# Kernel tuning notes

Measured on AMD Instinct MI355X. Metric: run time of the kernel, lower is better.

## Reference

```python
import jax, jax.numpy as jnp
import numpy as np

V, E, H, O = 50000, 300, 1024, 5
B, T = 64, 512


def setup_inputs() -> dict:
    key = jax.random.key(0)
    ks = jax.random.split(key, 8)
    s_ih = 1.0 / np.sqrt(H)
    return {
        "x": jax.random.randint(ks[0], (B, T), 0, V, dtype=jnp.int32),
        "embeddings": jax.random.normal(ks[1], (V, E), dtype=jnp.float32),
        "W_ih": jax.random.uniform(ks[2], (3 * H, E), jnp.float32, -s_ih, s_ih),
        "W_hh": jax.random.uniform(ks[3], (3 * H, H), jnp.float32, -s_ih, s_ih),
        "b_ih": jax.random.uniform(ks[4], (3 * H,), jnp.float32, -s_ih, s_ih),
        "b_hh": jax.random.uniform(ks[5], (3 * H,), jnp.float32, -s_ih, s_ih),
        "W_fc": jax.random.uniform(ks[6], (O, H), jnp.float32, -s_ih, s_ih),
        "b_fc": jax.random.uniform(ks[7], (O,), jnp.float32, -s_ih, s_ih),
    }


def _gru_last_hidden(emb, W_ih, W_hh, b_ih, b_hh):
    # emb: [B, T, E] -> last hidden state [B, H]
    Hd = W_hh.shape[1]
    # Precompute input contributions for all timesteps: [B, T, 3H]
    gx_all = jnp.einsum("bte,ge->btg", emb, W_ih) + b_ih
    gx_all = jnp.swapaxes(gx_all, 0, 1)  # [T, B, 3H] for scan

    def step(h, gx):
        gh = h @ W_hh.T + b_hh  # [B, 3H]
        xr, xz, xn = jnp.split(gx, 3, axis=-1)
        hr, hz, hn = jnp.split(gh, 3, axis=-1)
        r = jax.nn.sigmoid(xr + hr)
        z = jax.nn.sigmoid(xz + hz)
        n = jnp.tanh(xn + r * hn)
        h_new = (1.0 - z) * n + z * h
        return h_new, None

    h0 = jnp.zeros((emb.shape[0], Hd), dtype=emb.dtype)
    h_last, _ = jax.lax.scan(step, h0, gx_all)
    return h_last


def reference(x, embeddings, W_ih, W_hh, b_ih, b_hh, W_fc, b_fc):
    emb = embeddings[x]  # [B, T, E] embedding lookup (frozen table)
    h_last = _gru_last_hidden(emb, W_ih, W_hh, b_ih, b_hh)  # [B, H]
    return h_last @ W_fc.T + b_fc  # [B, O]
```

## Files before the change

kernel.cpp:

```cpp
#include <hip/hip_runtime.h>
#include <hip/hip_bf16.h>

typedef unsigned short u16;
typedef unsigned long long u64;
typedef __attribute__((ext_vector_type(8))) short bf16x8;
typedef __attribute__((ext_vector_type(4))) float f32x4;

#define MFMA16(a, b, c) __builtin_amdgcn_mfma_f32_16x16x32_bf16((a), (b), (c), 0, 0, 0)

static constexpr int Ee = 300, EP = 320, Hh = 1024, G3 = 3072;
static constexpr int Bb = 64, Tt = 512;

static constexpr long OFF_GX   = 0L;
static constexpr long OFF_EMB  = 201326592L;
static constexpr long OFF_WIH  = 222298112L;
static constexpr long OFF_WHH  = 224264192L;
static constexpr long OFF_HBUF = 230555648L;
static constexpr long OFF_FLAG = 230817792L;

__device__ __forceinline__ u16 f2bf(float f) {
    union { float f; unsigned u; } v; v.f = f;
    unsigned u = v.u;
    return (u16)((u + 0x7fffu + ((u >> 16) & 1u)) >> 16);
}
__device__ __forceinline__ float bf2f(u16 u) {
    union { unsigned u; float f; } v; v.u = ((unsigned)u) << 16;
    return v.f;
}
__device__ __forceinline__ float fast_sigmoid(float x) {
    return 1.f / (1.f + __expf(-x));
}
__device__ __forceinline__ float fast_tanh(float x) {
    float ax = fabsf(x);
    float e = __expf(-2.f * ax);
    float t = (1.f - e) / (1.f + e);
    return copysignf(t, x);
}

static constexpr long R0 = (long)Bb * Tt * EP;
static constexpr long R1 = (long)G3 * EP;
static constexpr long R2 = (long)G3 * Hh;
static constexpr long R3 = 131072;
static constexpr long R4 = 4096;
static constexpr long R5 = 320;

__global__ void prep_kernel(const int* __restrict__ x, const float* __restrict__ emb,
                            const float* __restrict__ wih, const float* __restrict__ whh,
                            const float* __restrict__ bfc,
                            u16* __restrict__ emb_bf, u16* __restrict__ wih_bf,
                            u16* __restrict__ whh_bf, u16* __restrict__ h0,
                            int* __restrict__ flags, float* __restrict__ out) {
    const long total = R0 + R1 + R2 + R3 + R4 + R5;
    for (long i = (long)blockIdx.x * blockDim.x + threadIdx.x; i < total;
         i += (long)gridDim.x * blockDim.x) {
        if (i < R0) {
            const int m = (int)(i / EP), k = (int)(i % EP);
            const int b = m & 63, t = m >> 6;
            u16 v = 0;
            if (k < Ee) {
                const int xi = x[b * Tt + t];
                v = f2bf(emb[(size_t)xi * Ee + k]);
            }
            emb_bf[i] = v;
        } else if (i < R0 + R1) {
            const long j = i - R0;
            const int k = (int)(j % EP);
            const int n = (int)(j / EP);
            wih_bf[j] = (k < Ee) ? f2bf(wih[(size_t)n * Ee + k]) : (u16)0;
        } else if (i < R0 + R1 + R2) {
            const long j = i - R0 - R1;
            whh_bf[j] = f2bf(whh[j]);
        } else if (i < R0 + R1 + R2 + R3) {
            h0[i - R0 - R1 - R2] = 0;
        } else if (i < R0 + R1 + R2 + R3 + R4) {
            flags[i - R0 - R1 - R2 - R3] = 0;
        } else {
            const long j = i - R0 - R1 - R2 - R3 - R4;
            out[j] = bfc[j % 5];
        }
    }
}

__global__ __launch_bounds__(256, 2)
void gx_gemm(const u16* __restrict__ A, const u16* __restrict__ Bm,
             const float* __restrict__ bih, u16* __restrict__ gx) {
    __shared__ __align__(16) u16 lA[128 * 32];
    __shared__ __align__(16) u16 lB[128 * 32];
    const int tid = threadIdx.x;
    const int lane = tid & 63;
    const int wv = tid >> 6;
    const int quad = lane >> 4, l15 = lane & 15;
    const int m0 = blockIdx.x * 128;
    const int n0 = blockIdx.y * 128;
    const int mo = (wv & 1) * 64, no = (wv >> 1) * 64;
    const int srow = tid >> 2;
    const int sseg = tid & 3;

    f32x4 acc[4][4] = {};

    for (int s = 0; s < 10; ++s) {
        const int k0 = s * 32;
        __syncthreads();
#pragma unroll
        for (int p = 0; p < 2; ++p) {
            const u16* ga = A + (size_t)(m0 + p * 64 + srow) * EP + k0 + sseg * 8;
            u16* la = &lA[p * 2048 + wv * 512];
            __builtin_amdgcn_global_load_lds(
                (const __attribute__((address_space(1))) void*)ga,
                (__attribute__((address_space(3))) void*)la, 16, 0, 0);
            const u16* gb = Bm + (size_t)(n0 + p * 64 + srow) * EP + k0 + sseg * 8;
            u16* lb = &lB[p * 2048 + wv * 512];
            __builtin_amdgcn_global_load_lds(
                (const __attribute__((address_space(1))) void*)gb,
                (__attribute__((address_space(3))) void*)lb, 16, 0, 0);
        }
        __syncthreads();

        bf16x8 af[4], bfr[4];
#pragma unroll
        for (int mt = 0; mt < 4; ++mt)
            af[mt] = *(const bf16x8*)&lA[(mo + mt * 16 + l15) * 32 + quad * 8];
#pragma unroll
        for (int nt = 0; nt < 4; ++nt)
            bfr[nt] = *(const bf16x8*)&lB[(no + nt * 16 + l15) * 32 + quad * 8];
#pragma unroll
        for (int mt = 0; mt < 4; ++mt)
#pragma unroll
            for (int nt = 0; nt < 4; ++nt)
                acc[mt][nt] = MFMA16(af[mt], bfr[nt], acc[mt][nt]);
    }

#pragma unroll
    for (int mt = 0; mt < 4; ++mt) {
        const int mg = m0 + mo + mt * 16 + quad * 4;
        const int t = mg >> 6, b0 = mg & 63;
#pragma unroll
        for (int nt = 0; nt < 4; ++nt) {
            const int n = n0 + no + nt * 16 + l15;
            const float bi = bih[n];
            ushort4 vv;
            vv.x = f2bf(acc[mt][nt][0] + bi);
            vv.y = f2bf(acc[mt][nt][1] + bi);
            vv.z = f2bf(acc[mt][nt][2] + bi);
            vv.w = f2bf(acc[mt][nt][3] + bi);
            *(ushort4*)&gx[((size_t)t * G3 + n) * 64 + b0] = vv;
        }
    }
}

__global__ __launch_bounds__(512, 2)
void scan_kernel(const u16* __restrict__ whh, const float* __restrict__ bhh,
                 const u16* __restrict__ gx, u16* __restrict__ hbuf,
                 const float* __restrict__ wfc, float* __restrict__ out,
                 int* __restrict__ flags) {
    __shared__ __align__(16) u16 lh[16 * 1032];
    __shared__ __align__(16) float red[2][3][4][16 * 20];

    const int bid = blockIdx.x;
    const int bg = bid >> 5;
    const int cg = bid & 31;
    const int w = threadIdx.x >> 6;
    const int lane = threadIdx.x & 63;
    const int kq = w & 3;
    const int nh = w >> 2;
    const int quad = lane >> 4, l15 = lane & 15;
    const int c0 = cg * 32;
    const bool isGate = (w == 3) || (w == 4);
    const int gnh = (w == 3) ? 0 : 1;

    bf16x8 wf[3][8];
#pragma unroll
    for (int g = 0; g < 3; ++g) {
        const size_t rbase = (size_t)(g * 1024 + c0 + nh * 16 + l15) * 1024;
#pragma unroll
        for (int s = 0; s < 8; ++s)
            wf[g][s] = *(const bf16x8*)&whh[rbase + (kq * 8 + s) * 32 + quad * 8];
    }

    float bh[3][4];
    u16 gxv[3][4];
    float hO[4] = {0.f, 0.f, 0.f, 0.f};
    if (isGate) {
#pragma unroll
        for (int g = 0; g < 3; ++g)
#pragma unroll
            for (int jj = 0; jj < 4; ++jj) {
                const int jglob = c0 + gnh * 16 + quad * 4 + jj;
                bh[g][jj] = bhh[g * 1024 + jglob];
                gxv[g][jj] = gx[((size_t)g * 1024 + jglob) * 64 + bg * 16 + l15];
            }
    }

    u64* hbq = (u64*)hbuf + (size_t)bg * 8192;
    int* gflag = &flags[(bg * 64 + lane) * 16];
    int* myflag = &flags[(bg * 64 + cg * 2 + gnh) * 16];
    const int srow = threadIdx.x >> 5;
    const int scol = threadIdx.x & 31;
    u64* lhq = (u64*)lh;

    for (int t = 0; t < 512; ++t) {
        const u64* hcq = hbq + (t & 1) * 4096;
        u16* hn = hbuf + (size_t)bg * 32768 + ((t + 1) & 1) * 16384;

        {
            int v = __hip_atomic_load(gflag, __ATOMIC_RELAXED, __HIP_MEMORY_SCOPE_AGENT);
            bool done = (v >= t);
            while (!__all(done)) {
                __builtin_amdgcn_s_sleep(1);
                if (!done) {
                    v = __hip_atomic_load(gflag, __ATOMIC_RELAXED, __HIP_MEMORY_SCOPE_AGENT);
                    done = (v >= t);
                }
            }
            __asm__ volatile("" ::: "memory");
        }

        u64 stg[8];
#pragma unroll
        for (int r = 0; r < 8; ++r)
            stg[r] = __hip_atomic_load(&hcq[srow * 256 + scol + 32 * r],
                                       __ATOMIC_RELAXED, __HIP_MEMORY_SCOPE_AGENT);
#pragma unroll
        for (int r = 0; r < 8; ++r)
            lhq[srow * 258 + scol + 32 * r] = stg[r];
        __syncthreads();

        bf16x8 af[8];
#pragma unroll
        for (int s = 0; s < 8; ++s)
            af[s] = *(const bf16x8*)&lh[l15 * 1032 + kq * 256 + s * 32 + quad * 8];
        f32x4 acc[3] = {};
#pragma unroll
        for (int s = 0; s < 8; ++s) {
            acc[0] = MFMA16(af[s], wf[0][s], acc[0]);
            acc[1] = MFMA16(af[s], wf[1][s], acc[1]);
            acc[2] = MFMA16(af[s], wf[2][s], acc[2]);
        }
#pragma unroll
        for (int g = 0; g < 3; ++g)
#pragma unroll
            for (int r = 0; r < 4; ++r)
                red[nh][g][kq][(quad * 4 + r) * 20 + l15] = acc[g][r];
        __syncthreads();

        if (isGate) {
            f32x4 rr[3][4];
#pragma unroll
            for (int g = 0; g < 3; ++g)
#pragma unroll
                for (int k = 0; k < 4; ++k)
                    rr[g][k] = *(const f32x4*)&red[gnh][g][k][l15 * 20 + quad * 4];
            u64 pack = 0;
#pragma unroll
            for (int jj = 0; jj < 4; ++jj) {
                const float s0 = rr[0][0][jj] + rr[0][1][jj] + rr[0][2][jj] + rr[0][3][jj];
                const float s1 = rr[1][0][jj] + rr[1][1][jj] + rr[1][2][jj] + rr[1][3][jj];
                const float s2 = rr[2][0][jj] + rr[2][1][jj] + rr[2][2][jj] + rr[2][3][jj];
                const float rg = fast_sigmoid(bf2f(gxv[0][jj]) + s0 + bh[0][jj]);
                const float zg = fast_sigmoid(bf2f(gxv[1][jj]) + s1 + bh[1][jj]);
                const float ng = fast_tanh(bf2f(gxv[2][jj]) + rg * (s2 + bh[2][jj]));
                const float hv = (1.f - zg) * ng + zg * hO[jj];
                hO[jj] = hv;
                pack |= (u64)f2bf(hv) << (jj * 16);
            }
            if (t < 511) {
                __hip_atomic_store((u64*)&hn[l15 * 1024 + c0 + gnh * 16 + quad * 4],
                                   pack, __ATOMIC_RELAXED, __HIP_MEMORY_SCOPE_AGENT);
                __builtin_amdgcn_s_waitcnt(0);
                if (lane == 0)
                    __hip_atomic_store(myflag, t + 1, __ATOMIC_RELAXED,
                                       __HIP_MEMORY_SCOPE_AGENT);
#pragma unroll
                for (int g = 0; g < 3; ++g)
#pragma unroll
                    for (int jj = 0; jj < 4; ++jj)
                        gxv[g][jj] = gx[((size_t)(t + 1) * G3 + g * 1024 + c0 +
                                         gnh * 16 + quad * 4 + jj) * 64 + bg * 16 + l15];
            }
        }
    }

    if (isGate) {
#pragma unroll
        for (int p = 0; p < 5; ++p) {
            float v = 0.f;
#pragma unroll
            for (int jj = 0; jj < 4; ++jj)
                v += hO[jj] * wfc[p * 1024 + c0 + gnh * 16 + quad * 4 + jj];
            v += __shfl_xor(v, 16);
            v += __shfl_xor(v, 32);
            if (quad == 0)
                atomicAdd(&out[(bg * 16 + l15) * 5 + p], v);
        }
    }
}

extern "C" void kernel_launch(void* const* d_in, const int* in_sizes, int n_in,
                              void* d_out, int out_size, void* d_ws, size_t ws_size,
                              hipStream_t stream) {
    const int*   x   = (const int*)d_in[0];
    const float* emb = (const float*)d_in[1];
    const float* wih = (const float*)d_in[2];
    const float* whh = (const float*)d_in[3];
    const float* bih = (const float*)d_in[4];
    const float* bhh = (const float*)d_in[5];
    const float* wfc = (const float*)d_in[6];
    const float* bfc = (const float*)d_in[7];
    float* out = (float*)d_out;

    char* ws = (char*)d_ws;
    u16*   gxw   = (u16*)(ws + OFF_GX);
    u16*   embbf = (u16*)(ws + OFF_EMB);
    u16*   wihbf = (u16*)(ws + OFF_WIH);
    u16*   whhbf = (u16*)(ws + OFF_WHH);
    u16*   hbuf  = (u16*)(ws + OFF_HBUF);
    int*   flags = (int*)(ws + OFF_FLAG);

    prep_kernel<<<8192, 256, 0, stream>>>(x, emb, wih, whh, bfc, embbf, wihbf,
                                          whhbf, hbuf, flags, out);

    gx_gemm<<<dim3(256, 24), 256, 0, stream>>>(embbf, wihbf, bih, gxw);

    scan_kernel<<<128, 512, 0, stream>>>(whhbf, bhh, gxw, hbuf, wfc, out, flags);
}
```

Baseline: 2.103 ms.

## Replace per-step flag barrier with timestep-tagged hidden-state words

Removes the separate flag array and its spin-wait. Each hidden value is now stored as a 32-bit word holding the bf16 value and the timestep tag, and consumers poll the data itself with coherent wide loads until every tag matches. This drops the store→waitcnt→flag-store→flag-load round trip from the critical serial path of the recurrence. In exchange the hidden-state traffic doubles and the tag/compare work runs on every poll.

```diff
diff --git a/kernel.cpp b/kernel.cpp
--- a/kernel.cpp
+++ b/kernel.cpp
@@ -2,9 +2,11 @@
 #include <hip/hip_bf16.h>
 
 typedef unsigned short u16;
+typedef unsigned int u32;
 typedef unsigned long long u64;
 typedef __attribute__((ext_vector_type(8))) short bf16x8;
 typedef __attribute__((ext_vector_type(4))) float f32x4;
+typedef __attribute__((ext_vector_type(4))) unsigned int u32x4;
 
 #define MFMA16(a, b, c) __builtin_amdgcn_mfma_f32_16x16x32_bf16((a), (b), (c), 0, 0, 0)
 
@@ -16,7 +18,6 @@
 static constexpr long OFF_WIH  = 222298112L;
 static constexpr long OFF_WHH  = 224264192L;
 static constexpr long OFF_HBUF = 230555648L;
-static constexpr long OFF_FLAG = 230817792L;
 
 __device__ __forceinline__ u16 f2bf(float f) {
     union { float f; unsigned u; } v; v.f = f;
@@ -41,16 +42,15 @@
 static constexpr long R1 = (long)G3 * EP;
 static constexpr long R2 = (long)G3 * Hh;
 static constexpr long R3 = 131072;
-static constexpr long R4 = 4096;
 static constexpr long R5 = 320;
 
 __global__ void prep_kernel(const int* __restrict__ x, const float* __restrict__ emb,
                             const float* __restrict__ wih, const float* __restrict__ whh,
                             const float* __restrict__ bfc,
                             u16* __restrict__ emb_bf, u16* __restrict__ wih_bf,
-                            u16* __restrict__ whh_bf, u16* __restrict__ h0,
-                            int* __restrict__ flags, float* __restrict__ out) {
-    const long total = R0 + R1 + R2 + R3 + R4 + R5;
+                            u16* __restrict__ whh_bf, u32* __restrict__ h32,
+                            float* __restrict__ out) {
+    const long total = R0 + R1 + R2 + R3 + R5;
     for (long i = (long)blockIdx.x * blockDim.x + threadIdx.x; i < total;
          i += (long)gridDim.x * blockDim.x) {
         if (i < R0) {
@@ -71,11 +71,10 @@
             const long j = i - R0 - R1;
             whh_bf[j] = f2bf(whh[j]);
         } else if (i < R0 + R1 + R2 + R3) {
-            h0[i - R0 - R1 - R2] = 0;
-        } else if (i < R0 + R1 + R2 + R3 + R4) {
-            flags[i - R0 - R1 - R2 - R3] = 0;
+            const long j = i - R0 - R1 - R2;
+            h32[j] = ((j >> 14) & 1) ? 0xFFFFu : 0u;
         } else {
-            const long j = i - R0 - R1 - R2 - R3 - R4;
+            const long j = i - R0 - R1 - R2 - R3;
             out[j] = bfc[j % 5];
         }
     }
@@ -150,17 +149,17 @@
 
 __global__ __launch_bounds__(512, 2)
 void scan_kernel(const u16* __restrict__ whh, const float* __restrict__ bhh,
-                 const u16* __restrict__ gx, u16* __restrict__ hbuf,
-                 const float* __restrict__ wfc, float* __restrict__ out,
-                 int* __restrict__ flags) {
+                 const u16* __restrict__ gx, u32* __restrict__ hball,
+                 const float* __restrict__ wfc, float* __restrict__ out) {
     __shared__ __align__(16) u16 lh[16 * 1032];
     __shared__ __align__(16) float red[2][3][4][16 * 20];
 
     const int bid = blockIdx.x;
     const int bg = bid >> 5;
     const int cg = bid & 31;
-    const int w = threadIdx.x >> 6;
-    const int lane = threadIdx.x & 63;
+    const int tid = threadIdx.x;
+    const int w = tid >> 6;
+    const int lane = tid & 63;
     const int kq = w & 3;
     const int nh = w >> 2;
     const int quad = lane >> 4, l15 = lane & 15;
@@ -191,38 +190,72 @@
             }
     }
 
-    u64* hbq = (u64*)hbuf + (size_t)bg * 8192;
-    int* gflag = &flags[(bg * 64 + lane) * 16];
-    int* myflag = &flags[(bg * 64 + cg * 2 + gnh) * 16];
-    const int srow = threadIdx.x >> 5;
-    const int scol = threadIdx.x & 31;
+    u32* hb = hball + (size_t)bg * 32768;
     u64* lhq = (u64*)lh;
+    const int t4 = tid << 2;
+    const int srow0 = tid >> 8;
+    const int sc4 = tid & 255;
 
     for (int t = 0; t < 512; ++t) {
-        const u64* hcq = hbq + (t & 1) * 4096;
-        u16* hn = hbuf + (size_t)bg * 32768 + ((t + 1) & 1) * 16384;
-
-        {
-            int v = __hip_atomic_load(gflag, __ATOMIC_RELAXED, __HIP_MEMORY_SCOPE_AGENT);
-            bool done = (v >= t);
-            while (!__all(done)) {
-                __builtin_amdgcn_s_sleep(1);
-                if (!done) {
-                    v = __hip_atomic_load(gflag, __ATOMIC_RELAXED, __HIP_MEMORY_SCOPE_AGENT);
-                    done = (v >= t);
-                }
-            }
-            __asm__ volatile("" ::: "memory");
-        }
-
-        u64 stg[8];
-#pragma unroll
-        for (int r = 0; r < 8; ++r)
-            stg[r] = __hip_atomic_load(&hcq[srow * 256 + scol + 32 * r],
-                                       __ATOMIC_RELAXED, __HIP_MEMORY_SCOPE_AGENT);
-#pragma unroll
-        for (int r = 0; r < 8; ++r)
-            lhq[srow * 258 + scol + 32 * r] = stg[r];
+        const u32* hs = hb + ((t & 1) << 14);
+        const u32 tg = (u32)t;
+
+        const u32* p0 = hs + t4;
+        const u32* p1 = hs + 2048 + t4;
+        const u32* p2 = hs + 4096 + t4;
+        const u32* p3 = hs + 6144 + t4;
+        const u32* p4 = hs + 8192 + t4;
+        const u32* p5 = hs + 10240 + t4;
+        const u32* p6 = hs + 12288 + t4;
+        const u32* p7 = hs + 14336 + t4;
+        u32x4 q0, q1, q2, q3, q4, q5, q6, q7;
+        for (;;) {
+            asm volatile(
+                "global_load_dwordx4 %0, %8, off sc0 sc1\n\t"
+                "global_load_dwordx4 %1, %9, off sc0 sc1\n\t"
+                "global_load_dwordx4 %2, %10, off sc0 sc1\n\t"
+                "global_load_dwordx4 %3, %11, off sc0 sc1\n\t"
+                "global_load_dwordx4 %4, %12, off sc0 sc1\n\t"
+                "global_load_dwordx4 %5, %13, off sc0 sc1\n\t"
+                "global_load_dwordx4 %6, %14, off sc0 sc1\n\t"
+                "global_load_dwordx4 %7, %15, off sc0 sc1\n\t"
+                "s_waitcnt vmcnt(0)"
+                : "=&v"(q0), "=&v"(q1), "=&v"(q2), "=&v"(q3),
+                  "=&v"(q4), "=&v"(q5), "=&v"(q6), "=&v"(q7)
+                : "v"(p0), "v"(p1), "v"(p2), "v"(p3),
+                  "v"(p4), "v"(p5), "v"(p6), "v"(p7)
+                : "memory");
+            bool ok = true;
+            ok &= ((q0.x & 0xffffu) == tg); ok &= ((q0.y & 0xffffu) == tg);
+            ok &= ((q0.z & 0xffffu) == tg); ok &= ((q0.w & 0xffffu) == tg);
+            ok &= ((q1.x & 0xffffu) == tg); ok &= ((q1.y & 0xffffu) == tg);
+            ok &= ((q1.z & 0xffffu) == tg); ok &= ((q1.w & 0xffffu) == tg);
+            ok &= ((q2.x & 0xffffu) == tg); ok &= ((q2.y & 0xffffu) == tg);
+            ok &= ((q2.z & 0xffffu) == tg); ok &= ((q2.w & 0xffffu) == tg);
+            ok &= ((q3.x & 0xffffu) == tg); ok &= ((q3.y & 0xffffu) == tg);
+            ok &= ((q3.z & 0xffffu) == tg); ok &= ((q3.w & 0xffffu) == tg);
+            ok &= ((q4.x & 0xffffu) == tg); ok &= ((q4.y & 0xffffu) == tg);
+            ok &= ((q4.z & 0xffffu) == tg); ok &= ((q4.w & 0xffffu) == tg);
+            ok &= ((q5.x & 0xffffu) == tg); ok &= ((q5.y & 0xffffu) == tg);
+            ok &= ((q5.z & 0xffffu) == tg); ok &= ((q5.w & 0xffffu) == tg);
+            ok &= ((q6.x & 0xffffu) == tg); ok &= ((q6.y & 0xffffu) == tg);
+            ok &= ((q6.z & 0xffffu) == tg); ok &= ((q6.w & 0xffffu) == tg);
+            ok &= ((q7.x & 0xffffu) == tg); ok &= ((q7.y & 0xffffu) == tg);
+            ok &= ((q7.z & 0xffffu) == tg); ok &= ((q7.w & 0xffffu) == tg);
+            if (__all(ok)) break;
+            __builtin_amdgcn_s_sleep(1);
+        }
+
+#define UNPK(rr, qq)                                                          \
+        {                                                                     \
+            const int row = (rr) * 2 + srow0;                                 \
+            const u32 lo = (qq.x >> 16) | (qq.y & 0xffff0000u);               \
+            const u32 hi = (qq.z >> 16) | (qq.w & 0xffff0000u);               \
+            lhq[row * 258 + sc4] = (u64)lo | ((u64)hi << 32);                 \
+        }
+        UNPK(0, q0) UNPK(1, q1) UNPK(2, q2) UNPK(3, q3)
+        UNPK(4, q4) UNPK(5, q5) UNPK(6, q6) UNPK(7, q7)
+#undef UNPK
         __syncthreads();
 
         bf16x8 af[8];
@@ -250,7 +283,7 @@
 #pragma unroll
                 for (int k = 0; k < 4; ++k)
                     rr[g][k] = *(const f32x4*)&red[gnh][g][k][l15 * 20 + quad * 4];
-            u64 pack = 0;
+            u32 wtag[4];
 #pragma unroll
             for (int jj = 0; jj < 4; ++jj) {
                 const float s0 = rr[0][0][jj] + rr[0][1][jj] + rr[0][2][jj] + rr[0][3][jj];
@@ -261,15 +294,17 @@
                 const float ng = fast_tanh(bf2f(gxv[2][jj]) + rg * (s2 + bh[2][jj]));
                 const float hv = (1.f - zg) * ng + zg * hO[jj];
                 hO[jj] = hv;
-                pack |= (u64)f2bf(hv) << (jj * 16);
+                wtag[jj] = ((u32)f2bf(hv) << 16) | (u32)(t + 1);
             }
             if (t < 511) {
-                __hip_atomic_store((u64*)&hn[l15 * 1024 + c0 + gnh * 16 + quad * 4],
-                                   pack, __ATOMIC_RELAXED, __HIP_MEMORY_SCOPE_AGENT);
-                __builtin_amdgcn_s_waitcnt(0);
-                if (lane == 0)
-                    __hip_atomic_store(myflag, t + 1, __ATOMIC_RELAXED,
-                                       __HIP_MEMORY_SCOPE_AGENT);
+                u32* hn = hb + (((t + 1) & 1) << 14);
+                const int widx = (l15 << 10) + c0 + gnh * 16 + (quad << 2);
+                __hip_atomic_store((u64*)&hn[widx],
+                                   (u64)wtag[0] | ((u64)wtag[1] << 32),
+                                   __ATOMIC_RELAXED, __HIP_MEMORY_SCOPE_AGENT);
+                __hip_atomic_store((u64*)&hn[widx + 2],
+                                   (u64)wtag[2] | ((u64)wtag[3] << 32),
+                                   __ATOMIC_RELAXED, __HIP_MEMORY_SCOPE_AGENT);
 #pragma unroll
                 for (int g = 0; g < 3; ++g)
 #pragma unroll
@@ -313,13 +348,12 @@
     u16*   embbf = (u16*)(ws + OFF_EMB);
     u16*   wihbf = (u16*)(ws + OFF_WIH);
     u16*   whhbf = (u16*)(ws + OFF_WHH);
-    u16*   hbuf  = (u16*)(ws + OFF_HBUF);
-    int*   flags = (int*)(ws + OFF_FLAG);
+    u32*   h32   = (u32*)(ws + OFF_HBUF);
 
     prep_kernel<<<8192, 256, 0, stream>>>(x, emb, wih, whh, bfc, embbf, wihbf,
-                                          whhbf, hbuf, flags, out);
+                                          whhbf, h32, out);
 
     gx_gemm<<<dim3(256, 24), 256, 0, stream>>>(embbf, wihbf, bih, gxw);
 
-    scan_kernel<<<128, 512, 0, stream>>>(whhbf, bhh, gxw, hbuf, wfc, out, flags);
-}
+    scan_kernel<<<128, 512, 0, stream>>>(whhbf, bhh, gxw, h32, wfc, out);
+}
```

New measurement: 2.408 ms. +14.5%, slower.
